# Kernel optimization log

Measured on AMD Instinct MI355X. Metric: run time of the kernel, lower is better.

The kernel has to match this reference:

```python
import jax, jax.numpy as jnp
import numpy as np

FS = 512.0
T = 2048
CYC_PHA, CYC_AMP = 3, 6
NBINS = 18
PHA_BANDS = [(2.0 + 2.0 * k, 4.0 + 2.0 * k) for k in range(10)]
AMP_BANDS = [(30.0 + 12.0 * k, 42.0 + 12.0 * k) for k in range(10)]


def _design_filter(fs, low, high, cycle):
    # windowed-sinc bandpass, taps = cycle * fs / low (tensorpac cycle rule), forced odd
    n = int(cycle * fs / low)
    if n % 2 == 0:
        n += 1
    t = np.arange(n) - (n - 1) / 2.0
    lp = lambda fc: 2.0 * fc / fs * np.sinc(2.0 * fc / fs * t)
    h = (lp(high) - lp(low)) * np.hamming(n)
    fc = 0.5 * (low + high)
    h = h / np.abs(np.sum(h * np.exp(-2j * np.pi * fc / fs * t)))  # unit gain at band center
    return h.astype(np.float32)


def _build_kernels():
    filts = [_design_filter(FS, l, h, CYC_PHA) for l, h in PHA_BANDS] + \
            [_design_filter(FS, l, h, CYC_AMP) for l, h in AMP_BANDS]
    L = max(f.shape[0] for f in filts)
    padded = []
    for f in filts:
        p = L - f.shape[0]
        pl = p // 2
        padded.append(np.pad(f, (pl, p - pl)))
    return np.stack(padded)  # (F, L), L odd


def _conv_same(sig, kernels):
    # sig: (N, Tp), kernels: (F, L) -> (N, F, Tp); cross-correlation, 'same' padding (L odd)
    L = kernels.shape[1]
    pad = (L - 1) // 2
    return jax.lax.conv_general_dilated(
        sig[:, None, :], kernels[:, None, :], window_strides=(1,),
        padding=((pad, L - 1 - pad),), dimension_numbers=("NCH", "OIH", "NCH"))


def _analytic(x):
    # FFT-based Hilbert analytic signal along last axis
    n = x.shape[-1]
    h = np.zeros(n, np.float32)
    h[0] = 1.0
    if n % 2 == 0:
        h[n // 2] = 1.0
        h[1:n // 2] = 2.0
    else:
        h[1:(n + 1) // 2] = 2.0
    return jnp.fft.ifft(jnp.fft.fft(x, axis=-1) * h, axis=-1)


def _modulation_index(pha, amp):
    # Tort MI: pha (B,C,P,S,T), amp (B,C,A,S,T) -> (B,C,P,A)
    idx = jnp.clip(jnp.floor((pha + jnp.pi) / (2.0 * jnp.pi) * NBINS), 0, NBINS - 1).astype(jnp.int32)
    sums, cnts = [], []
    for b in range(NBINS):  # fixed small bin count
        m = (idx == b).astype(amp.dtype)                       # (B,C,P,S,T)
        sums.append(jnp.einsum('bcpst,bcast->bcpas', m, amp))  # (B,C,P,A,S)
        cnts.append(m.sum(-1))                                 # (B,C,P,S)
    amp_sum = jnp.stack(sums, -1)                              # (B,C,P,A,S,N)
    cnt = jnp.stack(cnts, -1)[:, :, :, None, :, :]             # (B,C,P,1,S,N)
    amp_mean = amp_sum / jnp.maximum(cnt, 1.0)
    p = amp_mean / jnp.maximum(amp_mean.sum(-1, keepdims=True), 1e-12)
    log_n = jnp.log(jnp.asarray(NBINS, amp.dtype))
    mi = (log_n + (p * jnp.log(jnp.maximum(p, 1e-12))).sum(-1)) / log_n
    return mi.mean(-1)  # average over segments


def setup_inputs() -> dict:
    key = jax.random.key(0)
    x = jax.random.normal(key, (4, 8, 4, T), dtype=jnp.float32)
    kernels = jnp.asarray(_build_kernels())
    return {"x": x, "kernels": kernels}


def reference(x, kernels):
    B, C, S, Tlen = x.shape
    npha = len(PHA_BANDS)
    pad = kernels.shape[1] - 1  # max_padlen (edge_mode)
    sig = x.reshape(B * C * S, Tlen)
    sig = jnp.pad(sig, ((0, 0), (pad, pad)), mode='reflect')
    # filtfilt_mode: average forward conv and time-reversed conv
    fwd = _conv_same(sig, kernels)
    bwd = _conv_same(sig[:, ::-1], kernels)[:, :, ::-1]
    filt = 0.5 * (fwd + bwd)
    filt = filt[:, :, pad:-pad]  # strip edge padding -> (N, F, T)
    ana = _analytic(filt)
    pha = jnp.arctan2(ana.imag[:, :npha], ana.real[:, :npha])
    amp = jnp.sqrt(ana.real[:, npha:] ** 2 + ana.imag[:, npha:] ** 2)
    pha = pha.reshape(B, C, npha, S, Tlen)
    amp = amp.reshape(B, C, len(AMP_BANDS), S, Tlen)
    return _modulation_index(pha, amp)
```

## Files before the change

### kernel.cpp

```cpp
#include <hip/hip_runtime.h>
#include <math.h>

#define TT 2048
#define LK 769
#define NF 20
#define NS 128
#define NB 18
#define NFFT 4096

typedef __attribute__((ext_vector_type(8))) short short8;
typedef __attribute__((ext_vector_type(4))) float f32x4;

__device__ __forceinline__ float2 cmul(float2 a, float2 b) {
  return make_float2(a.x * b.x - a.y * b.y, a.x * b.y + a.y * b.x);
}
__device__ __forceinline__ float2 cmulc(float2 a, float2 b) {
  return make_float2(a.x * b.x + a.y * b.y, a.y * b.x - a.x * b.y);
}
#define CADD(a, b) make_float2((a).x + (b).x, (a).y + (b).y)
#define CSUB(a, b) make_float2((a).x - (b).x, (a).y - (b).y)

__device__ __forceinline__ void fwd_r8(float2* z, const float2* __restrict__ tw,
                                       int tt, int Q) {
  const float C = 0.70710678118654752f;
  const int j = tt & (Q - 1);
  const int base = ((tt & ~(Q - 1)) << 3) + j;
  const float2 x0 = z[base],         x1 = z[base + Q];
  const float2 x2 = z[base + 2 * Q], x3 = z[base + 3 * Q];
  const float2 x4 = z[base + 4 * Q], x5 = z[base + 5 * Q];
  const float2 x6 = z[base + 6 * Q], x7 = z[base + 7 * Q];
  const float2 W1 = tw[4 * Q + j], W2 = tw[2 * Q + j], W4 = tw[Q + j];
  const float2 W3 = cmul(W1, W2);
  const float2 W5 = cmul(W1, W4);
  const float2 W6 = cmul(W2, W4);
  const float2 W7 = cmul(W3, W4);
  const float2 s0 = CADD(x0, x4), s1 = CSUB(x0, x4);
  const float2 s2 = CADD(x2, x6), s3 = CSUB(x2, x6);
  const float2 E0 = CADD(s0, s2), E2 = CSUB(s0, s2);
  const float2 E1 = make_float2(s1.x + s3.y, s1.y - s3.x);
  const float2 E3 = make_float2(s1.x - s3.y, s1.y + s3.x);
  const float2 t0 = CADD(x1, x5), t1 = CSUB(x1, x5);
  const float2 t2 = CADD(x3, x7), t3 = CSUB(x3, x7);
  const float2 O0 = CADD(t0, t2), O2 = CSUB(t0, t2);
  const float2 O1 = make_float2(t1.x + t3.y, t1.y - t3.x);
  const float2 O3 = make_float2(t1.x - t3.y, t1.y + t3.x);
  const float2 wO1 = make_float2(C * (O1.x + O1.y), C * (O1.y - O1.x));
  const float2 w3O3 = make_float2(C * (O3.y - O3.x), -C * (O3.x + O3.y));
  const float2 mO2 = make_float2(O2.y, -O2.x);
  const float2 y0 = CADD(E0, O0), y4 = CSUB(E0, O0);
  const float2 y1 = CADD(E1, wO1), y5 = CSUB(E1, wO1);
  const float2 y2 = CADD(E2, mO2), y6 = CSUB(E2, mO2);
  const float2 y3 = CADD(E3, w3O3), y7 = CSUB(E3, w3O3);
  z[base]         = y0;
  z[base + Q]     = cmul(y1, W1);
  z[base + 2 * Q] = cmul(y2, W2);
  z[base + 3 * Q] = cmul(y3, W3);
  z[base + 4 * Q] = cmul(y4, W4);
  z[base + 5 * Q] = cmul(y5, W5);
  z[base + 6 * Q] = cmul(y6, W6);
  z[base + 7 * Q] = cmul(y7, W7);
}

__device__ __forceinline__ void fwd_r8_j0(float2* z, int base) {
  const float C = 0.70710678118654752f;
  const float2 x0 = z[base],     x1 = z[base + 1];
  const float2 x2 = z[base + 2], x3 = z[base + 3];
  const float2 x4 = z[base + 4], x5 = z[base + 5];
  const float2 x6 = z[base + 6], x7 = z[base + 7];
  const float2 s0 = CADD(x0, x4), s1 = CSUB(x0, x4);
  const float2 s2 = CADD(x2, x6), s3 = CSUB(x2, x6);
  const float2 E0 = CADD(s0, s2), E2 = CSUB(s0, s2);
  const float2 E1 = make_float2(s1.x + s3.y, s1.y - s3.x);
  const float2 E3 = make_float2(s1.x - s3.y, s1.y + s3.x);
  const float2 t0 = CADD(x1, x5), t1 = CSUB(x1, x5);
  const float2 t2 = CADD(x3, x7), t3 = CSUB(x3, x7);
  const float2 O0 = CADD(t0, t2), O2 = CSUB(t0, t2);
  const float2 O1 = make_float2(t1.x + t3.y, t1.y - t3.x);
  const float2 O3 = make_float2(t1.x - t3.y, t1.y + t3.x);
  const float2 wO1 = make_float2(C * (O1.x + O1.y), C * (O1.y - O1.x));
  const float2 w3O3 = make_float2(C * (O3.y - O3.x), -C * (O3.x + O3.y));
  const float2 mO2 = make_float2(O2.y, -O2.x);
  z[base]     = CADD(E0, O0);
  z[base + 4] = CSUB(E0, O0);
  z[base + 1] = CADD(E1, wO1);
  z[base + 5] = CSUB(E1, wO1);
  z[base + 2] = CADD(E2, mO2);
  z[base + 6] = CSUB(E2, mO2);
  z[base + 3] = CADD(E3, w3O3);
  z[base + 7] = CSUB(E3, w3O3);
}

__device__ __forceinline__ void inv_r8(float2* z, const float2* __restrict__ tw,
                                       int tt, int Q) {
  const float C = 0.70710678118654752f;
  const int j = tt & (Q - 1);
  const int base = ((tt & ~(Q - 1)) << 3) + j;
  const float2 W1 = tw[4 * Q + j], W2 = tw[2 * Q + j], W4 = tw[Q + j];
  const float2 W3 = cmul(W1, W2);
  const float2 W5 = cmul(W1, W4);
  const float2 W6 = cmul(W2, W4);
  const float2 W7 = cmul(W3, W4);
  const float2 u0 = z[base];
  const float2 u1 = cmulc(z[base + Q], W1);
  const float2 u2 = cmulc(z[base + 2 * Q], W2);
  const float2 u3 = cmulc(z[base + 3 * Q], W3);
  const float2 u4 = cmulc(z[base + 4 * Q], W4);
  const float2 u5 = cmulc(z[base + 5 * Q], W5);
  const float2 u6 = cmulc(z[base + 6 * Q], W6);
  const float2 u7 = cmulc(z[base + 7 * Q], W7);
  const float2 s0 = CADD(u0, u4), s1 = CSUB(u0, u4);
  const float2 s2 = CADD(u2, u6), s3 = CSUB(u2, u6);
  const float2 E0 = CADD(s0, s2), E2 = CSUB(s0, s2);
  const float2 E1 = make_float2(s1.x - s3.y, s1.y + s3.x);
  const float2 E3 = make_float2(s1.x + s3.y, s1.y - s3.x);
  const float2 t0 = CADD(u1, u5), t1 = CSUB(u1, u5);
  const float2 t2 = CADD(u3, u7), t3 = CSUB(u3, u7);
  const float2 O0 = CADD(t0, t2), O2 = CSUB(t0, t2);
  const float2 O1 = make_float2(t1.x - t3.y, t1.y + t3.x);
  const float2 O3 = make_float2(t1.x + t3.y, t1.y - t3.x);
  const float2 nO1 = make_float2(C * (O1.x - O1.y), C * (O1.x + O1.y));
  const float2 n3O3 = make_float2(-C * (O3.x + O3.y), C * (O3.x - O3.y));
  const float2 iO2 = make_float2(-O2.y, O2.x);
  z[base]         = CADD(E0, O0);
  z[base + 4 * Q] = CSUB(E0, O0);
  z[base + Q]     = CADD(E1, nO1);
  z[base + 5 * Q] = CSUB(E1, nO1);
  z[base + 2 * Q] = CADD(E2, iO2);
  z[base + 6 * Q] = CSUB(E2, iO2);
  z[base + 3 * Q] = CADD(E3, n3O3);
  z[base + 7 * Q] = CSUB(E3, n3O3);
}

__device__ __forceinline__ void inv8_j0_fused(float2* z,
                                              const float2* __restrict__ Xn,
                                              const float2* __restrict__ H1,
                                              const float2* __restrict__ H2,
                                              int b8) {
  const float4* X4 = (const float4*)(Xn + b8);
  const float4* A4 = (const float4*)(H1 + b8);
  const float4* B4 = (const float4*)(H2 + b8);
  float2 u[8];
#pragma unroll
  for (int q = 0; q < 4; ++q) {
    float4 xv = X4[q], av = A4[q], bv = B4[q];
    float2 Cc0 = make_float2(av.x - bv.y, av.y + bv.x);
    float2 Cc1 = make_float2(av.z - bv.w, av.w + bv.z);
    u[2 * q]     = cmul(make_float2(xv.x, xv.y), Cc0);
    u[2 * q + 1] = cmul(make_float2(xv.z, xv.w), Cc1);
  }
  const float C = 0.70710678118654752f;
  const float2 s0 = CADD(u[0], u[4]), s1 = CSUB(u[0], u[4]);
  const float2 s2 = CADD(u[2], u[6]), s3 = CSUB(u[2], u[6]);
  const float2 E0 = CADD(s0, s2), E2 = CSUB(s0, s2);
  const float2 E1 = make_float2(s1.x - s3.y, s1.y + s3.x);
  const float2 E3 = make_float2(s1.x + s3.y, s1.y - s3.x);
  const float2 t0 = CADD(u[1], u[5]), t1 = CSUB(u[1], u[5]);
  const float2 t2 = CADD(u[3], u[7]), t3 = CSUB(u[3], u[7]);
  const float2 O0 = CADD(t0, t2), O2 = CSUB(t0, t2);
  const float2 O1 = make_float2(t1.x - t3.y, t1.y + t3.x);
  const float2 O3 = make_float2(t1.x + t3.y, t1.y - t3.x);
  const float2 nO1 = make_float2(C * (O1.x - O1.y), C * (O1.x + O1.y));
  const float2 n3O3 = make_float2(-C * (O3.x + O3.y), C * (O3.x - O3.y));
  const float2 iO2 = make_float2(-O2.y, O2.x);
  z[b8]     = CADD(E0, O0);
  z[b8 + 4] = CSUB(E0, O0);
  z[b8 + 1] = CADD(E1, nO1);
  z[b8 + 5] = CSUB(E1, nO1);
  z[b8 + 2] = CADD(E2, iO2);
  z[b8 + 6] = CSUB(E2, iO2);
  z[b8 + 3] = CADD(E3, n3O3);
  z[b8 + 7] = CSUB(E3, n3O3);
}

__global__ __launch_bounds__(256) void prep_kernel(float2* __restrict__ tw,
                                                   float* __restrict__ out) {
  const int i = blockIdx.x * 256 + threadIdx.x;
  if (i == 0) {
    tw[0] = make_float2(1.f, 0.f);
  } else {
    int half = 1 << (31 - __clz(i));
    int j = i - half;
    float ang = -3.14159265358979323846f * (float)j / (float)half;
    float s, c;
    sincosf(ang, &s, &c);
    tw[i] = make_float2(c, s);
  }
  if (i < 3200) out[i] = 0.f;
}

__global__ __launch_bounds__(256) void specf_kernel(const float* __restrict__ x,
                                                    const float* __restrict__ ker,
                                                    const float2* __restrict__ tw,
                                                    float2* __restrict__ Hc,
                                                    float2* __restrict__ Xs) {
  __shared__ __align__(16) float2 z[NFFT];
  const int tid = threadIdx.x;
  const int blk = blockIdx.x;
  if (blk < NF) {
    const float* kr = ker + blk * LK;
#pragma unroll
    for (int h = 0; h < 16; ++h) {
      int i = tid + 256 * h;
      float v = 0.f;
      if (i < LK) v = 0.5f * (kr[i] + kr[LK - 1 - i]);
      z[i] = make_float2(v, 0.f);
    }
  } else {
    const float* xr = x + (size_t)(blk - NF) * TT;
#pragma unroll
    for (int h = 0; h < 16; ++h) {
      int i = tid + 256 * h;
      float v = 0.f;
      if (i < 2816) {
        int m = i - 384;
        if (m < 0) m = -m;
        if (m > 2047) m = 4094 - m;
        v = xr[m];
      }
      z[i] = make_float2(v, 0.f);
    }
  }
  __syncthreads();
  fwd_r8(z, tw, tid, 512);
  fwd_r8(z, tw, tid + 256, 512);
  __syncthreads();
  fwd_r8(z, tw, tid, 64);
  fwd_r8(z, tw, tid + 256, 64);
  __builtin_amdgcn_wave_barrier();
  fwd_r8(z, tw, tid, 8);
  fwd_r8(z, tw, tid + 256, 8);
  __builtin_amdgcn_wave_barrier();
  fwd_r8_j0(z, tid << 3);
  fwd_r8_j0(z, (tid + 256) << 3);
  __syncthreads();
  if (blk < NF) {
    const float s = 1.0f / 4096.0f;
    float2* o = Hc + (size_t)blk * NFFT;
#pragma unroll
    for (int h = 0; h < 16; ++h) {
      int i = tid + 256 * h;
      float2 v = z[i];
      o[i] = make_float2(v.x * s, -v.y * s);
    }
  } else {
    float2* o = Xs + (size_t)(blk - NF) * NFFT;
#pragma unroll
    for (int h = 0; h < 16; ++h) {
      int i = tid + 256 * h;
      o[i] = z[i];
    }
  }
}

__global__ __launch_bounds__(256) void convhil_kernel(const float2* __restrict__ Xs,
                                                      const float2* __restrict__ Hc,
                                                      const float2* __restrict__ tw,
                                                      float* __restrict__ filt,
                                                      unsigned int* __restrict__ binp) {
  __shared__ __align__(16) float2 z[NFFT];
  const int tid = threadIdx.x;
  const int wv = tid >> 6;
  const int lane = tid & 63;
  const int ord = blockIdx.x;
  const int p = ord / NS;
  const int n = ord % NS;
  const int o1 = p;
  const int o2 = 10 + (9 - p);
  const float2* Xn = Xs + (size_t)n * NFFT;
  const float2* H1 = Hc + (size_t)o1 * NFFT;
  const float2* H2 = Hc + (size_t)o2 * NFFT;
  inv8_j0_fused(z, Xn, H1, H2, tid << 3);
  inv8_j0_fused(z, Xn, H1, H2, (tid + 256) << 3);
  __builtin_amdgcn_wave_barrier();
  inv_r8(z, tw, tid, 8);
  inv_r8(z, tw, tid + 256, 8);
  __builtin_amdgcn_wave_barrier();
  inv_r8(z, tw, tid, 64);
  inv_r8(z, tw, tid + 256, 64);
  __syncthreads();
  inv_r8(z, tw, tid, 512);
  inv_r8(z, tw, tid + 256, 512);
  __syncthreads();
  const int bA = 4 * tid;
  const int bB = 1024 + 4 * tid;
  float acc1A[4], acc1B[4], acc2A[4], acc2B[4];
#pragma unroll
  for (int r = 0; r < 4; ++r) {
    float2 vA = z[bA + r]; acc1A[r] = vA.x; acc2A[r] = vA.y;
    float2 vB = z[bB + r]; acc1B[r] = vB.x; acc2B[r] = vB.y;
  }
  __syncthreads();
  fwd_r8(z, tw, tid, 256);
  __syncthreads();
  fwd_r8(z, tw, tid, 32);
  __builtin_amdgcn_wave_barrier();
  fwd_r8(z, tw, tid, 4);
  __builtin_amdgcn_wave_barrier();
#pragma unroll
  for (int h = 0; h < 2; ++h) {
    const int bf = 128 * wv + lane + 64 * h;
    const int base = bf << 2;
    const float2 x0 = z[base], x1 = z[base + 1];
    const float2 x2 = z[base + 2], x3 = z[base + 3];
    const float2 t0 = CADD(x0, x2), t1 = CSUB(x0, x2);
    const float2 t2 = CADD(x1, x3), t3 = CSUB(x1, x3);
    z[base]     = CADD(t0, t2);
    z[base + 1] = make_float2(t1.x + t3.y, t1.y - t3.x);
    z[base + 2] = CSUB(t0, t2);
    z[base + 3] = make_float2(t1.x - t3.y, t1.y + t3.x);
  }
  __builtin_amdgcn_wave_barrier();
#pragma unroll
  for (int i = 0; i < 8; ++i) {
    const int pp = 512 * wv + lane + 64 * i;
    if (pp != 0 && pp != 2) {
      if (pp & 2) { z[pp] = make_float2(0.f, 0.f); }
      else        { float2 v = z[pp]; z[pp] = make_float2(2.f * v.x, 2.f * v.y); }
    }
  }
  __builtin_amdgcn_wave_barrier();
#pragma unroll
  for (int h = 0; h < 2; ++h) {
    const int bf = 128 * wv + lane + 64 * h;
    const int base = bf << 2;
    const float2 u0 = z[base], u1 = z[base + 1];
    const float2 u2 = z[base + 2], u3 = z[base + 3];
    const float2 t0 = CADD(u0, u2), t1 = CSUB(u0, u2);
    const float2 t2 = CADD(u1, u3), t3 = CSUB(u1, u3);
    z[base]     = CADD(t0, t2);
    z[base + 1] = make_float2(t1.x - t3.y, t1.y + t3.x);
    z[base + 2] = CSUB(t0, t2);
    z[base + 3] = make_float2(t1.x + t3.y, t1.y - t3.x);
  }
  __builtin_amdgcn_wave_barrier();
  inv_r8(z, tw, tid, 4);
  __builtin_amdgcn_wave_barrier();
  inv_r8(z, tw, tid, 32);
  __builtin_amdgcn_wave_barrier();
  __syncthreads();
  inv_r8(z, tw, tid, 256);
  __syncthreads();
  unsigned int* bp = binp + ((size_t)n * 10 + o1) * 512;
  float* out2 = filt + ((size_t)n * NF + o2) * TT;
  const float invN = 1.0f / 2048.0f;
  float amA[4], amB[4];
  unsigned int dA = 0, dB = 0;
#pragma unroll
  for (int r = 0; r < 4; ++r) {
    float2 wvA = z[bA + r];
    float h1 = wvA.y * invN - acc2A[r];
    float h2 = acc1A[r] - wvA.x * invN;
    float phA = atan2f(h1, acc1A[r]);
    amA[r] = sqrtf(fmaf(acc2A[r], acc2A[r], h2 * h2));
    int b = (int)floorf((phA + 3.14159274f) / 6.2831855f * 18.0f);
    b = b < 0 ? 0 : (b > 17 ? 17 : b);
    dA |= ((unsigned int)b) << (8 * r);
    float2 wvB = z[bB + r];
    float g1 = wvB.y * invN - acc2B[r];
    float g2 = acc1B[r] - wvB.x * invN;
    float phB = atan2f(g1, acc1B[r]);
    amB[r] = sqrtf(fmaf(acc2B[r], acc2B[r], g2 * g2));
    int b2 = (int)floorf((phB + 3.14159274f) / 6.2831855f * 18.0f);
    b2 = b2 < 0 ? 0 : (b2 > 17 ? 17 : b2);
    dB |= ((unsigned int)b2) << (8 * r);
  }
  bp[tid] = dA;
  bp[tid + 256] = dB;
  *(float4*)&out2[bA] = make_float4(amA[0], amA[1], amA[2], amA[3]);
  *(float4*)&out2[bB] = make_float4(amB[0], amB[1], amB[2], amB[3]);
}

__global__ __launch_bounds__(256) void mi_kernel(const float* __restrict__ filt,
                                                 const unsigned int* __restrict__ binp,
                                                 float* __restrict__ out) {
  __shared__ __align__(16) unsigned int idxA[512], idxB[512];
  __shared__ float Cp[2][4][12][19];
  const int tid = threadIdx.x;
  const int wave = tid >> 6;
  const int lane = tid & 63;
  const int bid = blockIdx.x;
  const int blk = (bid & 7) * 80 + (bid >> 3);
  const int bc = blk / 20, r = blk % 20;
  const int jpA = r, jpB = r + 20;
  const unsigned int* bpA =
      binp + ((size_t)(bc * 4 + jpA / 10) * 10 + (jpA % 10)) * 512;
  const unsigned int* bpB =
      binp + ((size_t)(bc * 4 + jpB / 10) * 10 + (jpB % 10)) * 512;
  idxA[tid] = bpA[tid];
  idxA[tid + 256] = bpA[tid + 256];
  idxB[tid] = bpB[tid];
  idxB[tid + 256] = bpB[tid + 256];
  __syncthreads();
  const int n16 = lane & 15;
  const int quad = lane >> 4;
  const int aband = n16 < 10 ? n16 : 9;
  const int ja = (jpA & 3) + 4 * aband;
  const float* aptr = filt + ((size_t)(bc * 4 + ja / 10) * NF + 10 + (ja % 10)) * TT
                      + quad * 8;
  const bool isAmp = (n16 < 10);
  const bool isOne = (n16 == 10);
  f32x4 accA0 = {0.f, 0.f, 0.f, 0.f}, accA1 = {0.f, 0.f, 0.f, 0.f};
  f32x4 accB0 = {0.f, 0.f, 0.f, 0.f}, accB1 = {0.f, 0.f, 0.f, 0.f};
  const int s0 = wave * 16, s1 = s0 + 16;
  float4 p0 = make_float4(0.f, 0.f, 0.f, 0.f), p1 = p0;
  if (isAmp) {
    p0 = *(const float4*)(aptr + s0 * 32);
    p1 = *(const float4*)(aptr + s0 * 32 + 4);
  }
  for (int s = s0; s < s1; ++s) {
    float4 c0 = p0, c1 = p1;
    if (isAmp && s < s1 - 1) {
      p0 = *(const float4*)(aptr + (s + 1) * 32);
      p1 = *(const float4*)(aptr + (s + 1) * 32 + 4);
    }
    float a[8] = {c0.x, c0.y, c0.z, c0.w, c1.x, c1.y, c1.z, c1.w};
    short8 ah, am_, al;
#pragma unroll
    for (int j = 0; j < 8; ++j) {
      float v = isAmp ? a[j] : (isOne ? 1.0f : 0.0f);
      unsigned int u = __float_as_uint(v);
      float h = __uint_as_float(u & 0xFFFF0000u);
      float r1 = v - h;
      unsigned int u2 = __float_as_uint(r1);
      float md = __uint_as_float(u2 & 0xFFFF0000u);
      float r2 = r1 - md;
      unsigned int u3 = __float_as_uint(r2);
      ah[j] = (short)(u >> 16);
      am_[j] = (short)(u2 >> 16);
      al[j] = (short)(u3 >> 16);
    }
    const int dw = s * 8 + quad * 2;
    unsigned int dA0 = idxA[dw], dA1 = idxA[dw + 1];
    unsigned int dB0 = idxB[dw], dB1 = idxB[dw + 1];
    short8 bA0, bA1, bB0, bB1;
#pragma unroll
    for (int j = 0; j < 8; ++j) {
      unsigned int byA = ((j < 4 ? dA0 : dA1) >> ((j & 3) * 8)) & 0xFFu;
      unsigned int byB = ((j < 4 ? dB0 : dB1) >> ((j & 3) * 8)) & 0xFFu;
      bA0[j] = (byA == (unsigned int)n16) ? (short)0x3F80 : (short)0;
      bA1[j] = (byA == (unsigned int)(n16 + 16)) ? (short)0x3F80 : (short)0;
      bB0[j] = (byB == (unsigned int)n16) ? (short)0x3F80 : (short)0;
      bB1[j] = (byB == (unsigned int)(n16 + 16)) ? (short)0x3F80 : (short)0;
    }
    accA0 = __builtin_amdgcn_mfma_f32_16x16x32_bf16(ah, bA0, accA0, 0, 0, 0);
    accA0 = __builtin_amdgcn_mfma_f32_16x16x32_bf16(am_, bA0, accA0, 0, 0, 0);
    accA0 = __builtin_amdgcn_mfma_f32_16x16x32_bf16(al, bA0, accA0, 0, 0, 0);
    accA1 = __builtin_amdgcn_mfma_f32_16x16x32_bf16(ah, bA1, accA1, 0, 0, 0);
    accA1 = __builtin_amdgcn_mfma_f32_16x16x32_bf16(am_, bA1, accA1, 0, 0, 0);
    accA1 = __builtin_amdgcn_mfma_f32_16x16x32_bf16(al, bA1, accA1, 0, 0, 0);
    accB0 = __builtin_amdgcn_mfma_f32_16x16x32_bf16(ah, bB0, accB0, 0, 0, 0);
    accB0 = __builtin_amdgcn_mfma_f32_16x16x32_bf16(am_, bB0, accB0, 0, 0, 0);
    accB0 = __builtin_amdgcn_mfma_f32_16x16x32_bf16(al, bB0, accB0, 0, 0, 0);
    accB1 = __builtin_amdgcn_mfma_f32_16x16x32_bf16(ah, bB1, accB1, 0, 0, 0);
    accB1 = __builtin_amdgcn_mfma_f32_16x16x32_bf16(am_, bB1, accB1, 0, 0, 0);
    accB1 = __builtin_amdgcn_mfma_f32_16x16x32_bf16(al, bB1, accB1, 0, 0, 0);
  }
#pragma unroll
  for (int rr = 0; rr < 4; ++rr) {
    int row = quad * 4 + rr;
    if (row < 11) {
      Cp[0][wave][row][n16] = accA0[rr];
      Cp[1][wave][row][n16] = accB0[rr];
      if (n16 < 2) {
        Cp[0][wave][row][16 + n16] = accA1[rr];
        Cp[1][wave][row][16 + n16] = accB1[rr];
      }
    }
  }
  __syncthreads();
  int pl = -1, a_ = 0, jp_ = 0;
  if (tid < 10) { pl = 0; a_ = tid; jp_ = jpA; }
  else if (tid >= 64 && tid < 74) { pl = 1; a_ = tid - 64; jp_ = jpB; }
  if (pl >= 0) {
    float tot = 0.f, mb_[18];
#pragma unroll
    for (int b = 0; b < 18; ++b) {
      float s = Cp[pl][0][a_][b] + Cp[pl][1][a_][b] + Cp[pl][2][a_][b] + Cp[pl][3][a_][b];
      float c = Cp[pl][0][10][b] + Cp[pl][1][10][b] + Cp[pl][2][10][b] + Cp[pl][3][10][b];
      float mb = s / fmaxf(c, 1.0f);
      mb_[b] = mb; tot += mb;
    }
    tot = fmaxf(tot, 1e-12f);
    float s = 0.f;
#pragma unroll
    for (int b = 0; b < 18; ++b) {
      float pb = mb_[b] / tot;
      s += pb * logf(fmaxf(pb, 1e-12f));
    }
    const float LOGN = 2.8903717578961645f;
    atomicAdd(&out[bc * 100 + (jp_ >> 2) * 10 + a_],
              0.25f * (LOGN + s) / LOGN);
  }
}

extern "C" void kernel_launch(void* const* d_in, const int* in_sizes, int n_in,
                              void* d_out, int out_size, void* d_ws, size_t ws_size,
                              hipStream_t stream) {
  (void)in_sizes; (void)n_in; (void)out_size; (void)ws_size;
  const float* x = (const float*)d_in[0];
  const float* ker = (const float*)d_in[1];
  float* out = (float*)d_out;
  float* filt = (float*)d_ws;
  float2* tw = (float2*)(filt + (size_t)NS * NF * TT);
  float2* Hc = tw + NFFT;
  float2* Xs = Hc + (size_t)NF * NFFT;
  unsigned int* binp = (unsigned int*)(Xs + (size_t)NS * NFFT);

  prep_kernel<<<16, 256, 0, stream>>>(tw, out);
  specf_kernel<<<NF + NS, 256, 0, stream>>>(x, ker, tw, Hc, Xs);
  convhil_kernel<<<NS * 10, 256, 0, stream>>>(Xs, Hc, tw, filt, binp);
  mi_kernel<<<640, 256, 0, stream>>>(filt, binp, out);
}
```

Baseline: 123.7 us.

## Precompute FFT twiddles, pre-split amplitudes into bf16 triples, merge overflow-bin MFMAs

Three changes. First, a prep table of the derived radix-8 twiddles (W3, W5, W6, W7) is built once per stage, so the FFT butterflies load them instead of doing four complex multiplies each. Second, the conv/Hilbert kernel now stores amplitudes already split into hi/mid/lo bf16 parts in an MFMA-friendly interleaved layout, which moves the split out of the MI inner loop and changes the workspace layout. Third, the MI kernel packs the two overflow-bin accumulators (bins 16-17 for A and B) into one MFMA set, cutting MFMA count per step from 12 to 9.

```diff
diff --git a/kernel.cpp b/kernel.cpp
--- a/kernel.cpp
+++ b/kernel.cpp
@@ -8,8 +8,17 @@
 #define NB 18
 #define NFFT 4096
 
+#define TW3_Q4   0
+#define TW3_Q8   4
+#define TW3_Q32  12
+#define TW3_Q64  44
+#define TW3_Q256 108
+#define TW3_Q512 364
+#define TW3_TOT  876
+
 typedef __attribute__((ext_vector_type(8))) short short8;
 typedef __attribute__((ext_vector_type(4))) float f32x4;
+typedef __attribute__((ext_vector_type(4))) unsigned short us4;
 
 __device__ __forceinline__ float2 cmul(float2 a, float2 b) {
   return make_float2(a.x * b.x - a.y * b.y, a.x * b.y + a.y * b.x);
@@ -21,6 +30,7 @@
 #define CSUB(a, b) make_float2((a).x - (b).x, (a).y - (b).y)
 
 __device__ __forceinline__ void fwd_r8(float2* z, const float2* __restrict__ tw,
+                                       const float2* __restrict__ tw3q,
                                        int tt, int Q) {
   const float C = 0.70710678118654752f;
   const int j = tt & (Q - 1);
@@ -30,10 +40,12 @@
   const float2 x4 = z[base + 4 * Q], x5 = z[base + 5 * Q];
   const float2 x6 = z[base + 6 * Q], x7 = z[base + 7 * Q];
   const float2 W1 = tw[4 * Q + j], W2 = tw[2 * Q + j], W4 = tw[Q + j];
-  const float2 W3 = cmul(W1, W2);
-  const float2 W5 = cmul(W1, W4);
-  const float2 W6 = cmul(W2, W4);
-  const float2 W7 = cmul(W3, W4);
+  const float4 w35 = *(const float4*)(tw3q + 4 * j);
+  const float4 w67 = *(const float4*)(tw3q + 4 * j + 2);
+  const float2 W3 = make_float2(w35.x, w35.y);
+  const float2 W5 = make_float2(w35.z, w35.w);
+  const float2 W6 = make_float2(w67.x, w67.y);
+  const float2 W7 = make_float2(w67.z, w67.w);
   const float2 s0 = CADD(x0, x4), s1 = CSUB(x0, x4);
   const float2 s2 = CADD(x2, x6), s3 = CSUB(x2, x6);
   const float2 E0 = CADD(s0, s2), E2 = CSUB(s0, s2);
@@ -91,15 +103,18 @@
 }
 
 __device__ __forceinline__ void inv_r8(float2* z, const float2* __restrict__ tw,
+                                       const float2* __restrict__ tw3q,
                                        int tt, int Q) {
   const float C = 0.70710678118654752f;
   const int j = tt & (Q - 1);
   const int base = ((tt & ~(Q - 1)) << 3) + j;
   const float2 W1 = tw[4 * Q + j], W2 = tw[2 * Q + j], W4 = tw[Q + j];
-  const float2 W3 = cmul(W1, W2);
-  const float2 W5 = cmul(W1, W4);
-  const float2 W6 = cmul(W2, W4);
-  const float2 W7 = cmul(W3, W4);
+  const float4 w35 = *(const float4*)(tw3q + 4 * j);
+  const float4 w67 = *(const float4*)(tw3q + 4 * j + 2);
+  const float2 W3 = make_float2(w35.x, w35.y);
+  const float2 W5 = make_float2(w35.z, w35.w);
+  const float2 W6 = make_float2(w67.x, w67.y);
+  const float2 W7 = make_float2(w67.z, w67.w);
   const float2 u0 = z[base];
   const float2 u1 = cmulc(z[base + Q], W1);
   const float2 u2 = cmulc(z[base + 2 * Q], W2);
@@ -173,24 +188,57 @@
 }
 
 __global__ __launch_bounds__(256) void prep_kernel(float2* __restrict__ tw,
+                                                   float2* __restrict__ tw3,
                                                    float* __restrict__ out) {
-  const int i = blockIdx.x * 256 + threadIdx.x;
-  if (i == 0) {
-    tw[0] = make_float2(1.f, 0.f);
-  } else {
-    int half = 1 << (31 - __clz(i));
-    int j = i - half;
-    float ang = -3.14159265358979323846f * (float)j / (float)half;
-    float s, c;
-    sincosf(ang, &s, &c);
-    tw[i] = make_float2(c, s);
-  }
-  if (i < 3200) out[i] = 0.f;
+  const int blk = blockIdx.x;
+  const int tid = threadIdx.x;
+  if (blk < 16) {
+    const int i = blk * 256 + tid;
+    if (i == 0) {
+      tw[0] = make_float2(1.f, 0.f);
+    } else {
+      int half = 1 << (31 - __clz(i));
+      int j = i - half;
+      float ang = -3.14159265358979323846f * (float)j / (float)half;
+      float s, c;
+      sincosf(ang, &s, &c);
+      tw[i] = make_float2(c, s);
+    }
+    if (i < 3200) out[i] = 0.f;
+    return;
+  }
+  const int u = (blk - 16) * 256 + tid;
+  if (u >= TW3_TOT) return;
+  int Q, j;
+  if (u < TW3_Q8)        { Q = 4;   j = u; }
+  else if (u < TW3_Q32)  { Q = 8;   j = u - TW3_Q8; }
+  else if (u < TW3_Q64)  { Q = 32;  j = u - TW3_Q32; }
+  else if (u < TW3_Q256) { Q = 64;  j = u - TW3_Q64; }
+  else if (u < TW3_Q512) { Q = 256; j = u - TW3_Q256; }
+  else                   { Q = 512; j = u - TW3_Q512; }
+  const float PI = 3.14159265358979323846f;
+  float s, c;
+  float2 W1, W2, W4;
+  if (j == 0) { W1 = W2 = W4 = make_float2(1.f, 0.f); }
+  else {
+    float jf = (float)j;
+    sincosf(-PI * jf / (float)(4 * Q), &s, &c); W1 = make_float2(c, s);
+    sincosf(-PI * jf / (float)(2 * Q), &s, &c); W2 = make_float2(c, s);
+    sincosf(-PI * jf / (float)(Q),     &s, &c); W4 = make_float2(c, s);
+  }
+  float2 W3 = cmul(W1, W2);
+  float2 W5 = cmul(W1, W4);
+  float2 W6 = cmul(W2, W4);
+  float2 W7 = cmul(W3, W4);
+  float4* o = (float4*)(tw3 + 4 * (size_t)u);
+  o[0] = make_float4(W3.x, W3.y, W5.x, W5.y);
+  o[1] = make_float4(W6.x, W6.y, W7.x, W7.y);
 }
 
 __global__ __launch_bounds__(256) void specf_kernel(const float* __restrict__ x,
                                                     const float* __restrict__ ker,
                                                     const float2* __restrict__ tw,
+                                                    const float2* __restrict__ tw3,
                                                     float2* __restrict__ Hc,
                                                     float2* __restrict__ Xs) {
   __shared__ __align__(16) float2 z[NFFT];
@@ -221,14 +269,14 @@
     }
   }
   __syncthreads();
-  fwd_r8(z, tw, tid, 512);
-  fwd_r8(z, tw, tid + 256, 512);
-  __syncthreads();
-  fwd_r8(z, tw, tid, 64);
-  fwd_r8(z, tw, tid + 256, 64);
-  __builtin_amdgcn_wave_barrier();
-  fwd_r8(z, tw, tid, 8);
-  fwd_r8(z, tw, tid + 256, 8);
+  fwd_r8(z, tw, tw3 + 4 * TW3_Q512, tid, 512);
+  fwd_r8(z, tw, tw3 + 4 * TW3_Q512, tid + 256, 512);
+  __syncthreads();
+  fwd_r8(z, tw, tw3 + 4 * TW3_Q64, tid, 64);
+  fwd_r8(z, tw, tw3 + 4 * TW3_Q64, tid + 256, 64);
+  __builtin_amdgcn_wave_barrier();
+  fwd_r8(z, tw, tw3 + 4 * TW3_Q8, tid, 8);
+  fwd_r8(z, tw, tw3 + 4 * TW3_Q8, tid + 256, 8);
   __builtin_amdgcn_wave_barrier();
   fwd_r8_j0(z, tid << 3);
   fwd_r8_j0(z, (tid + 256) << 3);
@@ -255,7 +303,8 @@
 __global__ __launch_bounds__(256) void convhil_kernel(const float2* __restrict__ Xs,
                                                       const float2* __restrict__ Hc,
                                                       const float2* __restrict__ tw,
-                                                      float* __restrict__ filt,
+                                                      const float2* __restrict__ tw3,
+                                                      unsigned short* __restrict__ amps,
                                                       unsigned int* __restrict__ binp) {
   __shared__ __align__(16) float2 z[NFFT];
   const int tid = threadIdx.x;
@@ -272,14 +321,14 @@
   inv8_j0_fused(z, Xn, H1, H2, tid << 3);
   inv8_j0_fused(z, Xn, H1, H2, (tid + 256) << 3);
   __builtin_amdgcn_wave_barrier();
-  inv_r8(z, tw, tid, 8);
-  inv_r8(z, tw, tid + 256, 8);
-  __builtin_amdgcn_wave_barrier();
-  inv_r8(z, tw, tid, 64);
-  inv_r8(z, tw, tid + 256, 64);
-  __syncthreads();
-  inv_r8(z, tw, tid, 512);
-  inv_r8(z, tw, tid + 256, 512);
+  inv_r8(z, tw, tw3 + 4 * TW3_Q8, tid, 8);
+  inv_r8(z, tw, tw3 + 4 * TW3_Q8, tid + 256, 8);
+  __builtin_amdgcn_wave_barrier();
+  inv_r8(z, tw, tw3 + 4 * TW3_Q64, tid, 64);
+  inv_r8(z, tw, tw3 + 4 * TW3_Q64, tid + 256, 64);
+  __syncthreads();
+  inv_r8(z, tw, tw3 + 4 * TW3_Q512, tid, 512);
+  inv_r8(z, tw, tw3 + 4 * TW3_Q512, tid + 256, 512);
   __syncthreads();
   const int bA = 4 * tid;
   const int bB = 1024 + 4 * tid;
@@ -290,11 +339,11 @@
     float2 vB = z[bB + r]; acc1B[r] = vB.x; acc2B[r] = vB.y;
   }
   __syncthreads();
-  fwd_r8(z, tw, tid, 256);
-  __syncthreads();
-  fwd_r8(z, tw, tid, 32);
-  __builtin_amdgcn_wave_barrier();
-  fwd_r8(z, tw, tid, 4);
+  fwd_r8(z, tw, tw3 + 4 * TW3_Q256, tid, 256);
+  __syncthreads();
+  fwd_r8(z, tw, tw3 + 4 * TW3_Q32, tid, 32);
+  __builtin_amdgcn_wave_barrier();
+  fwd_r8(z, tw, tw3 + 4 * TW3_Q4, tid, 4);
   __builtin_amdgcn_wave_barrier();
 #pragma unroll
   for (int h = 0; h < 2; ++h) {
@@ -333,17 +382,20 @@
     z[base + 3] = make_float2(t1.x + t3.y, t1.y - t3.x);
   }
   __builtin_amdgcn_wave_barrier();
-  inv_r8(z, tw, tid, 4);
-  __builtin_amdgcn_wave_barrier();
-  inv_r8(z, tw, tid, 32);
-  __builtin_amdgcn_wave_barrier();
-  __syncthreads();
-  inv_r8(z, tw, tid, 256);
+  inv_r8(z, tw, tw3 + 4 * TW3_Q4, tid, 4);
+  __builtin_amdgcn_wave_barrier();
+  inv_r8(z, tw, tw3 + 4 * TW3_Q32, tid, 32);
+  __builtin_amdgcn_wave_barrier();
+  __syncthreads();
+  inv_r8(z, tw, tw3 + 4 * TW3_Q256, tid, 256);
   __syncthreads();
   unsigned int* bp = binp + ((size_t)n * 10 + o1) * 512;
-  float* out2 = filt + ((size_t)n * NF + o2) * TT;
+  const int rid = n * 10 + (o2 - 10);
+  unsigned short* ap = amps + (size_t)rid * (TT * 3);
+  const int offA = (tid >> 1) * 24 + (tid & 1) * 4;
+  const int offB = (128 + (tid >> 1)) * 24 + (tid & 1) * 4;
   const float invN = 1.0f / 2048.0f;
-  float amA[4], amB[4];
+  us4 hA, mA, lA, hB, mB, lB;
   unsigned int dA = 0, dB = 0;
 #pragma unroll
   for (int r = 0; r < 4; ++r) {
@@ -351,7 +403,7 @@
     float h1 = wvA.y * invN - acc2A[r];
     float h2 = acc1A[r] - wvA.x * invN;
     float phA = atan2f(h1, acc1A[r]);
-    amA[r] = sqrtf(fmaf(acc2A[r], acc2A[r], h2 * h2));
+    float vA = sqrtf(fmaf(acc2A[r], acc2A[r], h2 * h2));
     int b = (int)floorf((phA + 3.14159274f) / 6.2831855f * 18.0f);
     b = b < 0 ? 0 : (b > 17 ? 17 : b);
     dA |= ((unsigned int)b) << (8 * r);
@@ -359,18 +411,46 @@
     float g1 = wvB.y * invN - acc2B[r];
     float g2 = acc1B[r] - wvB.x * invN;
     float phB = atan2f(g1, acc1B[r]);
-    amB[r] = sqrtf(fmaf(acc2B[r], acc2B[r], g2 * g2));
+    float vB = sqrtf(fmaf(acc2B[r], acc2B[r], g2 * g2));
     int b2 = (int)floorf((phB + 3.14159274f) / 6.2831855f * 18.0f);
     b2 = b2 < 0 ? 0 : (b2 > 17 ? 17 : b2);
     dB |= ((unsigned int)b2) << (8 * r);
+    {
+      unsigned int u = __float_as_uint(vA);
+      float hf = __uint_as_float(u & 0xFFFF0000u);
+      float r1 = vA - hf;
+      unsigned int u2 = __float_as_uint(r1);
+      float md = __uint_as_float(u2 & 0xFFFF0000u);
+      float r2 = r1 - md;
+      unsigned int u3 = __float_as_uint(r2);
+      hA[r] = (unsigned short)(u >> 16);
+      mA[r] = (unsigned short)(u2 >> 16);
+      lA[r] = (unsigned short)(u3 >> 16);
+    }
+    {
+      unsigned int u = __float_as_uint(vB);
+      float hf = __uint_as_float(u & 0xFFFF0000u);
+      float r1 = vB - hf;
+      unsigned int u2 = __float_as_uint(r1);
+      float md = __uint_as_float(u2 & 0xFFFF0000u);
+      float r2 = r1 - md;
+      unsigned int u3 = __float_as_uint(r2);
+      hB[r] = (unsigned short)(u >> 16);
+      mB[r] = (unsigned short)(u2 >> 16);
+      lB[r] = (unsigned short)(u3 >> 16);
+    }
   }
   bp[tid] = dA;
   bp[tid + 256] = dB;
-  *(float4*)&out2[bA] = make_float4(amA[0], amA[1], amA[2], amA[3]);
-  *(float4*)&out2[bB] = make_float4(amB[0], amB[1], amB[2], amB[3]);
-}
-
-__global__ __launch_bounds__(256) void mi_kernel(const float* __restrict__ filt,
+  *(us4*)(ap + offA)      = hA;
+  *(us4*)(ap + offA + 8)  = mA;
+  *(us4*)(ap + offA + 16) = lA;
+  *(us4*)(ap + offB)      = hB;
+  *(us4*)(ap + offB + 8)  = mB;
+  *(us4*)(ap + offB + 16) = lB;
+}
+
+__global__ __launch_bounds__(256) void mi_kernel(const unsigned short* __restrict__ amps,
                                                  const unsigned int* __restrict__ binp,
                                                  float* __restrict__ out) {
   __shared__ __align__(16) unsigned int idxA[512], idxB[512];
@@ -395,65 +475,55 @@
   const int quad = lane >> 4;
   const int aband = n16 < 10 ? n16 : 9;
   const int ja = (jpA & 3) + 4 * aband;
-  const float* aptr = filt + ((size_t)(bc * 4 + ja / 10) * NF + 10 + (ja % 10)) * TT
-                      + quad * 8;
+  const int nsig = bc * 4 + ja / 10;
+  const int rid = nsig * 10 + (ja % 10);
+  const unsigned short* aptr = amps + (size_t)rid * (TT * 3) + quad * 24;
   const bool isAmp = (n16 < 10);
   const bool isOne = (n16 == 10);
-  f32x4 accA0 = {0.f, 0.f, 0.f, 0.f}, accA1 = {0.f, 0.f, 0.f, 0.f};
-  f32x4 accB0 = {0.f, 0.f, 0.f, 0.f}, accB1 = {0.f, 0.f, 0.f, 0.f};
+  const int tgt1 = n16 < 2 ? n16 + 16 : (n16 < 4 ? n16 + 14 : 255);
+  const bool useA1 = (n16 < 2);
+  short8 aOne, aZero;
+#pragma unroll
+  for (int j = 0; j < 8; ++j) {
+    aOne[j] = isOne ? (short)0x3F80 : (short)0;
+    aZero[j] = 0;
+  }
+  f32x4 accA0 = {0.f, 0.f, 0.f, 0.f};
+  f32x4 accB0 = {0.f, 0.f, 0.f, 0.f};
+  f32x4 accC1 = {0.f, 0.f, 0.f, 0.f};
   const int s0 = wave * 16, s1 = s0 + 16;
-  float4 p0 = make_float4(0.f, 0.f, 0.f, 0.f), p1 = p0;
-  if (isAmp) {
-    p0 = *(const float4*)(aptr + s0 * 32);
-    p1 = *(const float4*)(aptr + s0 * 32 + 4);
-  }
   for (int s = s0; s < s1; ++s) {
-    float4 c0 = p0, c1 = p1;
-    if (isAmp && s < s1 - 1) {
-      p0 = *(const float4*)(aptr + (s + 1) * 32);
-      p1 = *(const float4*)(aptr + (s + 1) * 32 + 4);
-    }
-    float a[8] = {c0.x, c0.y, c0.z, c0.w, c1.x, c1.y, c1.z, c1.w};
-    short8 ah, am_, al;
-#pragma unroll
-    for (int j = 0; j < 8; ++j) {
-      float v = isAmp ? a[j] : (isOne ? 1.0f : 0.0f);
-      unsigned int u = __float_as_uint(v);
-      float h = __uint_as_float(u & 0xFFFF0000u);
-      float r1 = v - h;
-      unsigned int u2 = __float_as_uint(r1);
-      float md = __uint_as_float(u2 & 0xFFFF0000u);
-      float r2 = r1 - md;
-      unsigned int u3 = __float_as_uint(r2);
-      ah[j] = (short)(u >> 16);
-      am_[j] = (short)(u2 >> 16);
-      al[j] = (short)(u3 >> 16);
+    short8 ah, amv, alv;
+    if (isAmp) {
+      const unsigned short* g = aptr + s * 96;
+      ah  = *(const short8*)(g);
+      amv = *(const short8*)(g + 8);
+      alv = *(const short8*)(g + 16);
+    } else {
+      ah = aOne; amv = aZero; alv = aZero;
     }
     const int dw = s * 8 + quad * 2;
     unsigned int dA0 = idxA[dw], dA1 = idxA[dw + 1];
     unsigned int dB0 = idxB[dw], dB1 = idxB[dw + 1];
-    short8 bA0, bA1, bB0, bB1;
+    short8 bA0, bB0, bC1;
 #pragma unroll
     for (int j = 0; j < 8; ++j) {
       unsigned int byA = ((j < 4 ? dA0 : dA1) >> ((j & 3) * 8)) & 0xFFu;
       unsigned int byB = ((j < 4 ? dB0 : dB1) >> ((j & 3) * 8)) & 0xFFu;
       bA0[j] = (byA == (unsigned int)n16) ? (short)0x3F80 : (short)0;
-      bA1[j] = (byA == (unsigned int)(n16 + 16)) ? (short)0x3F80 : (short)0;
       bB0[j] = (byB == (unsigned int)n16) ? (short)0x3F80 : (short)0;
-      bB1[j] = (byB == (unsigned int)(n16 + 16)) ? (short)0x3F80 : (short)0;
-    }
-    accA0 = __builtin_amdgcn_mfma_f32_16x16x32_bf16(ah, bA0, accA0, 0, 0, 0);
-    accA0 = __builtin_amdgcn_mfma_f32_16x16x32_bf16(am_, bA0, accA0, 0, 0, 0);
-    accA0 = __builtin_amdgcn_mfma_f32_16x16x32_bf16(al, bA0, accA0, 0, 0, 0);
-    accA1 = __builtin_amdgcn_mfma_f32_16x16x32_bf16(ah, bA1, accA1, 0, 0, 0);
-    accA1 = __builtin_amdgcn_mfma_f32_16x16x32_bf16(am_, bA1, accA1, 0, 0, 0);
-    accA1 = __builtin_amdgcn_mfma_f32_16x16x32_bf16(al, bA1, accA1, 0, 0, 0);
-    accB0 = __builtin_amdgcn_mfma_f32_16x16x32_bf16(ah, bB0, accB0, 0, 0, 0);
-    accB0 = __builtin_amdgcn_mfma_f32_16x16x32_bf16(am_, bB0, accB0, 0, 0, 0);
-    accB0 = __builtin_amdgcn_mfma_f32_16x16x32_bf16(al, bB0, accB0, 0, 0, 0);
-    accB1 = __builtin_amdgcn_mfma_f32_16x16x32_bf16(ah, bB1, accB1, 0, 0, 0);
-    accB1 = __builtin_amdgcn_mfma_f32_16x16x32_bf16(am_, bB1, accB1, 0, 0, 0);
-    accB1 = __builtin_amdgcn_mfma_f32_16x16x32_bf16(al, bB1, accB1, 0, 0, 0);
+      unsigned int byC = useA1 ? byA : byB;
+      bC1[j] = (byC == (unsigned int)tgt1) ? (short)0x3F80 : (short)0;
+    }
+    accA0 = __builtin_amdgcn_mfma_f32_16x16x32_bf16(ah,  bA0, accA0, 0, 0, 0);
+    accA0 = __builtin_amdgcn_mfma_f32_16x16x32_bf16(amv, bA0, accA0, 0, 0, 0);
+    accA0 = __builtin_amdgcn_mfma_f32_16x16x32_bf16(alv, bA0, accA0, 0, 0, 0);
+    accB0 = __builtin_amdgcn_mfma_f32_16x16x32_bf16(ah,  bB0, accB0, 0, 0, 0);
+    accB0 = __builtin_amdgcn_mfma_f32_16x16x32_bf16(amv, bB0, accB0, 0, 0, 0);
+    accB0 = __builtin_amdgcn_mfma_f32_16x16x32_bf16(alv, bB0, accB0, 0, 0, 0);
+    accC1 = __builtin_amdgcn_mfma_f32_16x16x32_bf16(ah,  bC1, accC1, 0, 0, 0);
+    accC1 = __builtin_amdgcn_mfma_f32_16x16x32_bf16(amv, bC1, accC1, 0, 0, 0);
+    accC1 = __builtin_amdgcn_mfma_f32_16x16x32_bf16(alv, bC1, accC1, 0, 0, 0);
   }
 #pragma unroll
   for (int rr = 0; rr < 4; ++rr) {
@@ -461,10 +531,8 @@
     if (row < 11) {
       Cp[0][wave][row][n16] = accA0[rr];
       Cp[1][wave][row][n16] = accB0[rr];
-      if (n16 < 2) {
-        Cp[0][wave][row][16 + n16] = accA1[rr];
-        Cp[1][wave][row][16 + n16] = accB1[rr];
-      }
+      if (n16 < 2)      Cp[0][wave][row][16 + n16] = accC1[rr];
+      else if (n16 < 4) Cp[1][wave][row][14 + n16] = accC1[rr];
     }
   }
   __syncthreads();
@@ -500,14 +568,15 @@
   const float* x = (const float*)d_in[0];
   const float* ker = (const float*)d_in[1];
   float* out = (float*)d_out;
-  float* filt = (float*)d_ws;
-  float2* tw = (float2*)(filt + (size_t)NS * NF * TT);
-  float2* Hc = tw + NFFT;
-  float2* Xs = Hc + (size_t)NF * NFFT;
+  unsigned short* amps = (unsigned short*)d_ws;
+  float2* tw  = (float2*)(amps + (size_t)NS * 10 * TT * 3);
+  float2* tw3 = tw + NFFT;
+  float2* Hc  = tw3 + 4 * TW3_TOT;
+  float2* Xs  = Hc + (size_t)NF * NFFT;
   unsigned int* binp = (unsigned int*)(Xs + (size_t)NS * NFFT);
 
-  prep_kernel<<<16, 256, 0, stream>>>(tw, out);
-  specf_kernel<<<NF + NS, 256, 0, stream>>>(x, ker, tw, Hc, Xs);
-  convhil_kernel<<<NS * 10, 256, 0, stream>>>(Xs, Hc, tw, filt, binp);
-  mi_kernel<<<640, 256, 0, stream>>>(filt, binp, out);
-}
+  prep_kernel<<<20, 256, 0, stream>>>(tw, tw3, out);
+  specf_kernel<<<NF + NS, 256, 0, stream>>>(x, ker, tw, tw3, Hc, Xs);
+  convhil_kernel<<<NS * 10, 256, 0, stream>>>(Xs, Hc, tw, tw3, amps, binp);
+  mi_kernel<<<640, 256, 0, stream>>>(amps, binp, out);
+}
```

After: 123.7 us. Within noise of the previous version (-0.0%).
